# Kernel tuning notes

Hardware: AMD Instinct MI355X
Metric: run time of the kernel (lower is better)

Reference implementation:

```python
import jax, jax.numpy as jnp
import numpy as np

HID = 1024
INTER = 4096
NUM_EXPERTS = 4096
NUM_KEYS = 64  # floor(sqrt(4096))
TOP_K = 8
B, S = 2, 2048


def setup_inputs() -> dict:
    key = jax.random.key(0)
    ks = jax.random.split(key, 7)
    sc = 0.02
    return {
        "hidden_states": jax.random.normal(ks[0], (B, S, HID), jnp.float32),
        "w_gate": jax.random.normal(ks[1], (INTER, HID), jnp.float32) * sc,
        "w_up": jax.random.normal(ks[2], (INTER, HID), jnp.float32) * sc,
        "w_down": jax.random.normal(ks[3], (HID, INTER), jnp.float32) * sc,
        "w_router": jax.random.normal(ks[4], (NUM_KEYS * 2, HID), jnp.float32) * sc,
        "down_embed": jax.random.normal(ks[5], (NUM_EXPERTS, HID), jnp.float32) * sc,
        "up_embed": jax.random.normal(ks[6], (NUM_EXPERTS, HID), jnp.float32) * sc,
    }


def reference(hidden_states, w_gate, w_up, w_down, w_router, down_embed, up_embed):
    b, s, h = hidden_states.shape
    n = b * s
    # router: [b,s,2*nk] -> row-major reshape to (2, n, nk), matching torch .view
    router_logits = (hidden_states @ w_router.T).reshape(2, n, NUM_KEYS)
    # topk with k == nk is a full descending sort (faithful to torch .topk)
    scores_xy, idx_xy = jax.lax.top_k(router_logits, NUM_KEYS)
    scores_x, scores_y = scores_xy[0], scores_xy[1]  # (n, nk) each
    idx_x, idx_y = idx_xy[0], idx_xy[1]
    all_scores = (scores_x[:, :, None] + scores_y[:, None, :]).reshape(n, NUM_KEYS * NUM_KEYS)
    all_indices = (idx_x[:, :, None] * NUM_KEYS + idx_y[:, None, :]).reshape(n, NUM_KEYS * NUM_KEYS)
    scores, pos = jax.lax.top_k(all_scores, TOP_K)  # (n, top_k)
    indices = jnp.take_along_axis(all_indices, pos, axis=-1)
    routing_weights = jax.nn.softmax(scores, axis=-1)
    routing_weights = routing_weights / routing_weights.sum(-1, keepdims=True)  # norm_topk_prob
    de = down_embed[indices]  # (n, top_k, h)
    ue = up_embed[indices]    # (n, top_k, h)
    x_flat = hidden_states.reshape(n, h)
    ew = jnp.einsum('nkh,nh->nk', de, x_flat)
    ew = jax.nn.silu(ew) * routing_weights
    experts_states = jnp.einsum('nk,nkh->nh', ew, ue).reshape(b, s, h)
    mlp = (jax.nn.silu(x_flat @ w_gate.T) * (x_flat @ w_up.T)) @ w_down.T
    out = mlp.reshape(b, s, h) + experts_states
    return (out, router_logits)
```

## Files before the change

### kernel.cpp

```cpp
#include <hip/hip_runtime.h>
#include <hip/hip_bf16.h>
#include <stdint.h>

typedef __bf16 bf16;
typedef __attribute__((ext_vector_type(8))) __bf16 bf16x8;
typedef __attribute__((ext_vector_type(4))) float f32x4;

static constexpr int kTok = 4096;
static constexpr int kHid = 1024;
static constexpr int kInter = 4096;

#define GLDS16(g, l)                                                \
  __builtin_amdgcn_global_load_lds(                                 \
      (const __attribute__((address_space(1))) void*)(g),           \
      (__attribute__((address_space(3))) void*)(l), 16, 0, 0)

__global__ void __launch_bounds__(256) k_cvt_rt(
    const float* X, const float* Wg, const float* Wu, const float* Wd,
    const float* Wr, const float* dE, const float* uE,
    bf16* Xb, bf16* Wgb, bf16* Wub, bf16* Wdb, bf16* dEb, bf16* uEb,
    float* out1) {
  __shared__ bf16 smem[8192];
  const int bid = blockIdx.x;
  const int t = threadIdx.x;

  if (bid < 32) {
    const int w = t >> 6;
    const int L = t & 63;
    const int la = L & 15;
    const int lk = (L >> 4) * 8;
    bf16* sA = smem;
    bf16* sB = smem + 4096;
    const long m0 = (long)bid * 128;
    const int wm = (w >> 1) * 64;
    const int wn = (w & 1) * 64;
    const f32x4 fzero = {0.f, 0.f, 0.f, 0.f};
    f32x4 acc[4][4];
#pragma unroll
    for (int i = 0; i < 4; ++i)
#pragma unroll
      for (int j = 0; j < 4; ++j) acc[i][j] = fzero;

    const int c0 = t, c1 = t + 256;
    const long ar0 = m0 + (c0 >> 2), ar1 = m0 + (c1 >> 2);
    const long br0 = (c0 >> 2), br1 = (c1 >> 2);
    const int ko = (c0 & 3) * 8;
    const bf16* sAr = sA + (wm + la) * 32 + lk;
    const bf16* sBr = sB + (wn + la) * 32 + lk;

    for (int kt = 0; kt < 32; ++kt) {
      const long k0 = (long)kt << 5;
      bf16x8 av0, av1, bv0, bv1;
      {
        const f32x4 x0 = *(const f32x4*)(X + ar0 * kHid + k0 + ko);
        const f32x4 x1 = *(const f32x4*)(X + ar0 * kHid + k0 + ko + 4);
        const f32x4 y0 = *(const f32x4*)(X + ar1 * kHid + k0 + ko);
        const f32x4 y1 = *(const f32x4*)(X + ar1 * kHid + k0 + ko + 4);
        const f32x4 p0 = *(const f32x4*)(Wr + br0 * kHid + k0 + ko);
        const f32x4 p1 = *(const f32x4*)(Wr + br0 * kHid + k0 + ko + 4);
        const f32x4 q0 = *(const f32x4*)(Wr + br1 * kHid + k0 + ko);
        const f32x4 q1 = *(const f32x4*)(Wr + br1 * kHid + k0 + ko + 4);
#pragma unroll
        for (int i = 0; i < 4; ++i) {
          av0[i] = (bf16)x0[i]; av0[4 + i] = (bf16)x1[i];
          av1[i] = (bf16)y0[i]; av1[4 + i] = (bf16)y1[i];
          bv0[i] = (bf16)p0[i]; bv0[4 + i] = (bf16)p1[i];
          bv1[i] = (bf16)q0[i]; bv1[4 + i] = (bf16)q1[i];
        }
      }
      __syncthreads();
      *(bf16x8*)(sA + c0 * 8) = av0;
      *(bf16x8*)(sA + c1 * 8) = av1;
      *(bf16x8*)(sB + c0 * 8) = bv0;
      *(bf16x8*)(sB + c1 * 8) = bv1;
      __syncthreads();
      bf16x8 af[4], bfm[4];
#pragma unroll
      for (int i = 0; i < 4; ++i) {
        af[i] = *(const bf16x8*)(sAr + i * 512);
        bfm[i] = *(const bf16x8*)(sBr + i * 512);
      }
#pragma unroll
      for (int i = 0; i < 4; ++i)
#pragma unroll
        for (int j = 0; j < 4; ++j)
          acc[i][j] = __builtin_amdgcn_mfma_f32_16x16x32_bf16(
              af[i], bfm[j], acc[i][j], 0, 0, 0);
    }
    const long col0 = wn + la;
    const long row0 = m0 + wm + (L >> 4) * 4;
#pragma unroll
    for (int i = 0; i < 4; ++i)
#pragma unroll
      for (int j = 0; j < 4; ++j)
#pragma unroll
        for (int r = 0; r < 4; ++r)
          out1[(row0 + i * 16 + r) * 128 + col0 + j * 16] = acc[i][j][r];
    return;
  }

  if (bid >= 8224) {
    const int c2 = bid - 8224;
    const float* src = (c2 >> 11) ? uE : dE;
    bf16* dst = (c2 >> 11) ? uEb : dEb;
    const long i = ((long)(c2 & 2047) * 256 + t) * 8;
    const f32x4 a = *(const f32x4*)(src + i);
    const f32x4 b = *(const f32x4*)(src + i + 4);
    bf16x8 o;
#pragma unroll
    for (int k = 0; k < 4; ++k) { o[k] = (bf16)a[k]; o[4 + k] = (bf16)b[k]; }
    *(bf16x8*)(dst + i) = o;
    return;
  }

  const int c = bid - 32;
  const float* src;
  bf16* dst;
  switch (c >> 11) {
    case 0: src = X;  dst = Xb;  break;
    case 1: src = Wg; dst = Wgb; break;
    case 2: src = Wu; dst = Wub; break;
    default: src = Wd; dst = Wdb; break;
  }
  const long i = ((long)(c & 2047) * 256 + t) * 8;
  const f32x4 a = *(const f32x4*)(src + i);
  const f32x4 b = *(const f32x4*)(src + i + 4);
  bf16x8 o;
#pragma unroll
  for (int k = 0; k < 4; ++k) { o[k] = (bf16)a[k]; o[4 + k] = (bf16)b[k]; }
  *(bf16x8*)(dst + i) = o;
}

__global__ void __launch_bounds__(256, 2) gemm_gu(
    const bf16* X, const bf16* Wg, const bf16* Wu, bf16* H) {
  constexpr int K = kHid, N = kInter;
  __shared__ bf16 sX[128 * 32];
  __shared__ bf16 sG[128 * 32];
  __shared__ bf16 sU[128 * 32];
  const int t = threadIdx.x;
  const int w = t >> 6;
  const int L = t & 63;
  const long m0 = (long)blockIdx.y * 128;
  const long n0 = (long)blockIdx.x * 128;
  const int wm = (w >> 1) * 64;
  const int wn = (w & 1) * 64;

  f32x4 accG[4][4], accU[4][4];
  const f32x4 fzero = {0.f, 0.f, 0.f, 0.f};
#pragma unroll
  for (int i = 0; i < 4; ++i)
#pragma unroll
    for (int j = 0; j < 4; ++j) { accG[i][j] = fzero; accU[i][j] = fzero; }

  const int r0 = t >> 2;
  const int ko = (t & 3) * 8;
  const bf16* gX0 = X + (m0 + r0) * K + ko;
  const bf16* gX1 = gX0 + (long)64 * K;
  const bf16* gG0 = Wg + (n0 + r0) * K + ko;
  const bf16* gG1 = gG0 + (long)64 * K;
  const bf16* gU0 = Wu + (n0 + r0) * K + ko;
  const bf16* gU1 = gU0 + (long)64 * K;
  bf16* lX0 = sX + w * 512;
  bf16* lX1 = sX + 2048 + w * 512;
  bf16* lG0 = sG + w * 512;
  bf16* lG1 = sG + 2048 + w * 512;
  bf16* lU0 = sU + w * 512;
  bf16* lU1 = sU + 2048 + w * 512;

  const int la = L & 15;
  const int lk = (L >> 4) * 8;
  const bf16* sXr = sX + (wm + la) * 32 + lk;
  const bf16* sGr = sG + (wn + la) * 32 + lk;
  const bf16* sUr = sU + (wn + la) * 32 + lk;

  for (int kt = 0; kt < K / 32; ++kt) {
    const long k0 = (long)kt << 5;
    GLDS16(gX0 + k0, lX0);
    GLDS16(gX1 + k0, lX1);
    GLDS16(gG0 + k0, lG0);
    GLDS16(gG1 + k0, lG1);
    GLDS16(gU0 + k0, lU0);
    GLDS16(gU1 + k0, lU1);
    __syncthreads();
    bf16x8 af[4], bg[4], bu[4];
#pragma unroll
    for (int i = 0; i < 4; ++i) {
      af[i] = *(const bf16x8*)(sXr + i * 512);
      bg[i] = *(const bf16x8*)(sGr + i * 512);
      bu[i] = *(const bf16x8*)(sUr + i * 512);
    }
#pragma unroll
    for (int i = 0; i < 4; ++i)
#pragma unroll
      for (int j = 0; j < 4; ++j) {
        accG[i][j] = __builtin_amdgcn_mfma_f32_16x16x32_bf16(af[i], bg[j],
                                                             accG[i][j], 0, 0, 0);
        accU[i][j] = __builtin_amdgcn_mfma_f32_16x16x32_bf16(af[i], bu[j],
                                                             accU[i][j], 0, 0, 0);
      }
    __syncthreads();
  }
  const long col0 = n0 + wn + la;
  const long row0 = m0 + wm + (L >> 4) * 4;
#pragma unroll
  for (int i = 0; i < 4; ++i)
#pragma unroll
    for (int j = 0; j < 4; ++j)
#pragma unroll
      for (int r = 0; r < 4; ++r) {
        const float g = accG[i][j][r];
        const float u = accU[i][j][r];
        H[(row0 + i * 16 + r) * N + col0 + j * 16] =
            (bf16)(g / (1.f + __expf(-g)) * u);
      }
}

__global__ void __launch_bounds__(256, 2) gemm_down(
    const bf16* Hs, const bf16* Wd, float* out0, float* p1) {
  constexpr int K = kInter, N = kHid;
  __shared__ bf16 sA[128 * 32];
  __shared__ bf16 sB[128 * 32];
  const int t = threadIdx.x;
  const int w = t >> 6;
  const int L = t & 63;
  const long m0 = (long)blockIdx.y * 128;
  const long n0 = (long)blockIdx.x * 128;
  const long zb = (long)blockIdx.z * 2048;
  const int wm = (w >> 1) * 64;
  const int wn = (w & 1) * 64;

  f32x4 acc[4][4];
  const f32x4 fzero = {0.f, 0.f, 0.f, 0.f};
#pragma unroll
  for (int i = 0; i < 4; ++i)
#pragma unroll
    for (int j = 0; j < 4; ++j) acc[i][j] = fzero;

  const int r0 = t >> 2;
  const int ko = (t & 3) * 8;
  const bf16* gA0 = Hs + (m0 + r0) * K + zb + ko;
  const bf16* gA1 = gA0 + (long)64 * K;
  const bf16* gB0 = Wd + (n0 + r0) * K + zb + ko;
  const bf16* gB1 = gB0 + (long)64 * K;
  bf16* lA0 = sA + w * 512;
  bf16* lA1 = sA + 2048 + w * 512;
  bf16* lB0 = sB + w * 512;
  bf16* lB1 = sB + 2048 + w * 512;

  const int la = L & 15;
  const int lk = (L >> 4) * 8;
  const bf16* sAr = sA + (wm + la) * 32 + lk;
  const bf16* sBr = sB + (wn + la) * 32 + lk;

  for (int kt = 0; kt < 64; ++kt) {
    const long k0 = (long)kt << 5;
    GLDS16(gA0 + k0, lA0);
    GLDS16(gA1 + k0, lA1);
    GLDS16(gB0 + k0, lB0);
    GLDS16(gB1 + k0, lB1);
    __syncthreads();
    bf16x8 af[4], bfm[4];
#pragma unroll
    for (int i = 0; i < 4; ++i) {
      af[i] = *(const bf16x8*)(sAr + i * 512);
      bfm[i] = *(const bf16x8*)(sBr + i * 512);
    }
#pragma unroll
    for (int i = 0; i < 4; ++i)
#pragma unroll
      for (int j = 0; j < 4; ++j)
        acc[i][j] = __builtin_amdgcn_mfma_f32_16x16x32_bf16(af[i], bfm[j],
                                                            acc[i][j], 0, 0, 0);
    __syncthreads();
  }
  float* dst = (blockIdx.z == 0) ? out0 : p1;
  const long col0 = n0 + wn + la;
  const long row0 = m0 + wm + (L >> 4) * 4;
#pragma unroll
  for (int i = 0; i < 4; ++i)
#pragma unroll
    for (int j = 0; j < 4; ++j)
#pragma unroll
      for (int r = 0; r < 4; ++r)
        dst[(row0 + i * 16 + r) * N + col0 + j * 16] = acc[i][j][r];
}

template <int BT>
__global__ void __launch_bounds__(256) route_expert(
    const float* __restrict__ logits, const float* __restrict__ X,
    const float* __restrict__ dE, const float* __restrict__ uE,
    const bf16* __restrict__ dEb, const bf16* __restrict__ uEb,
    const float* __restrict__ p1, float* __restrict__ out0) {
  __shared__ float s_vals[2][128];
  __shared__ int s_idx[2][128];
  __shared__ float s_acc[2][16][64];
  const int w = threadIdx.x >> 6;
  const int L = threadIdx.x & 63;
  const int tok = w >> 1;
  const int h = w & 1;
  const int j = blockIdx.x * 2 + tok;

  const int half = (j & 1) * 64;
  const int rx = j >> 1;
  const float vx = logits[(long)rx * 128 + half + L];
  const float vy = logits[(long)(2048 + rx) * 128 + half + L];

  int rkx = 0, rky = 0;
  for (int m = 0; m < 64; ++m) {
    const float mx = __shfl(vx, m);
    const float my = __shfl(vy, m);
    rkx += (mx > vx) || (mx == vx && m < L);
    rky += (my > vy) || (my == vy && m < L);
  }
  rkx &= 63;
  rky &= 63;
  s_vals[tok][rkx] = vx;
  s_idx[tok][rkx] = L;
  s_vals[tok][64 + rky] = vy;
  s_idx[tok][64 + rky] = L;
  __syncthreads();

  int p = 0, q = 0;
  const bool valid = (L < 20);
  if (L < 8)       { p = L;      q = 0; }
  else if (L < 12) { p = L - 8;  q = 1; }
  else if (L < 14) { p = L - 12; q = 2; }
  else if (L < 16) { p = L - 14; q = 3; }
  else if (L < 20) { p = 0;      q = L - 12; }
  const float kNegBig = -3.0e38f;
  float myv = valid ? (s_vals[tok][p] + s_vals[tok][64 + q]) : kNegBig;
  int mypos = valid ? (p * 64 + q) : 0x7fffffff;

  float topv[8];
  int tope[8];
#pragma unroll
  for (int r = 0; r < 8; ++r) {
    float bv = myv;
    int bp = mypos;
#pragma unroll
    for (int d = 32; d > 0; d >>= 1) {
      const float ov = __shfl_xor(bv, d);
      const int op = __shfl_xor(bp, d);
      if (ov > bv || (ov == bv && op < bp)) { bv = ov; bp = op; }
    }
    topv[r] = bv;
    const int pp = (bp >> 6) & 127, qq = bp & 63;
    tope[r] = (s_idx[tok][pp] * 64 + s_idx[tok][64 + qq]) & 4095;
    if (mypos == bp) myv = kNegBig;
  }

  float e[8], wsum = 0.f;
#pragma unroll
  for (int r = 0; r < 8; ++r) {
    e[r] = __expf(topv[r] - topv[0]);
    wsum += e[r];
  }
  const float winv = 1.f / wsum;

  const long xoff = (long)j * kHid + L * 16;
  float xv[16], acc[16];
#pragma unroll
  for (int v4 = 0; v4 < 4; ++v4) {
    const f32x4 xl = *(const f32x4*)(X + xoff + v4 * 4);
#pragma unroll
    for (int i = 0; i < 4; ++i) { xv[v4 * 4 + i] = xl[i]; acc[v4 * 4 + i] = 0.f; }
  }

  const long lo16 = (long)L * 16;
  if (BT) {
    const long eo0 = (long)tope[h * 4 + 0] * kHid + lo16;
    const long eo1 = (long)tope[h * 4 + 1] * kHid + lo16;
    const long eo2 = (long)tope[h * 4 + 2] * kHid + lo16;
    const long eo3 = (long)tope[h * 4 + 3] * kHid + lo16;
    const bf16x8 d00 = *(const bf16x8*)(dEb + eo0);
    const bf16x8 d01 = *(const bf16x8*)(dEb + eo0 + 8);
    const bf16x8 d10 = *(const bf16x8*)(dEb + eo1);
    const bf16x8 d11 = *(const bf16x8*)(dEb + eo1 + 8);
    const bf16x8 d20 = *(const bf16x8*)(dEb + eo2);
    const bf16x8 d21 = *(const bf16x8*)(dEb + eo2 + 8);
    const bf16x8 d30 = *(const bf16x8*)(dEb + eo3);
    const bf16x8 d31 = *(const bf16x8*)(dEb + eo3 + 8);
    const bf16x8 u00 = *(const bf16x8*)(uEb + eo0);
    const bf16x8 u01 = *(const bf16x8*)(uEb + eo0 + 8);
    const bf16x8 u10 = *(const bf16x8*)(uEb + eo1);
    const bf16x8 u11 = *(const bf16x8*)(uEb + eo1 + 8);
    const bf16x8 u20 = *(const bf16x8*)(uEb + eo2);
    const bf16x8 u21 = *(const bf16x8*)(uEb + eo2 + 8);
    const bf16x8 u30 = *(const bf16x8*)(uEb + eo3);
    const bf16x8 u31 = *(const bf16x8*)(uEb + eo3 + 8);

    float d0 = 0.f, d1 = 0.f, d2 = 0.f, d3 = 0.f;
#pragma unroll
    for (int i = 0; i < 8; ++i) {
      d0 += (float)d00[i] * xv[i] + (float)d01[i] * xv[8 + i];
      d1 += (float)d10[i] * xv[i] + (float)d11[i] * xv[8 + i];
      d2 += (float)d20[i] * xv[i] + (float)d21[i] * xv[8 + i];
      d3 += (float)d30[i] * xv[i] + (float)d31[i] * xv[8 + i];
    }
#pragma unroll
    for (int dd = 32; dd > 0; dd >>= 1) {
      d0 += __shfl_xor(d0, dd);
      d1 += __shfl_xor(d1, dd);
      d2 += __shfl_xor(d2, dd);
      d3 += __shfl_xor(d3, dd);
    }
    const float w0 = d0 / (1.f + __expf(-d0)) * (e[h * 4 + 0] * winv);
    const float w1 = d1 / (1.f + __expf(-d1)) * (e[h * 4 + 1] * winv);
    const float w2 = d2 / (1.f + __expf(-d2)) * (e[h * 4 + 2] * winv);
    const float w3 = d3 / (1.f + __expf(-d3)) * (e[h * 4 + 3] * winv);
#pragma unroll
    for (int i = 0; i < 8; ++i) {
      acc[i]     += w0 * (float)u00[i] + w1 * (float)u10[i] +
                    w2 * (float)u20[i] + w3 * (float)u30[i];
      acc[8 + i] += w0 * (float)u01[i] + w1 * (float)u11[i] +
                    w2 * (float)u21[i] + w3 * (float)u31[i];
    }
  } else {
    long eoA = (long)tope[h * 4 + 0] * kHid + lo16;
    f32x4 dA0 = *(const f32x4*)(dE + eoA);
    f32x4 dA1 = *(const f32x4*)(dE + eoA + 4);
    f32x4 dA2 = *(const f32x4*)(dE + eoA + 8);
    f32x4 dA3 = *(const f32x4*)(dE + eoA + 12);
    f32x4 uA0 = *(const f32x4*)(uE + eoA);
    f32x4 uA1 = *(const f32x4*)(uE + eoA + 4);
    f32x4 uA2 = *(const f32x4*)(uE + eoA + 8);
    f32x4 uA3 = *(const f32x4*)(uE + eoA + 12);
#pragma unroll
    for (int r = 0; r < 4; ++r) {
      f32x4 dB0, dB1, dB2, dB3, uB0, uB1, uB2, uB3;
      if (r < 3) {
        const long eoB = (long)tope[h * 4 + r + 1] * kHid + lo16;
        dB0 = *(const f32x4*)(dE + eoB);
        dB1 = *(const f32x4*)(dE + eoB + 4);
        dB2 = *(const f32x4*)(dE + eoB + 8);
        dB3 = *(const f32x4*)(dE + eoB + 12);
        uB0 = *(const f32x4*)(uE + eoB);
        uB1 = *(const f32x4*)(uE + eoB + 4);
        uB2 = *(const f32x4*)(uE + eoB + 8);
        uB3 = *(const f32x4*)(uE + eoB + 12);
      }
      float d = 0.f;
#pragma unroll
      for (int i = 0; i < 4; ++i) {
        d += dA0[i] * xv[i];
        d += dA1[i] * xv[4 + i];
        d += dA2[i] * xv[8 + i];
        d += dA3[i] * xv[12 + i];
      }
#pragma unroll
      for (int dd = 32; dd > 0; dd >>= 1) d += __shfl_xor(d, dd);
      const float ew = d / (1.f + __expf(-d)) * (e[h * 4 + r] * winv);
#pragma unroll
      for (int i = 0; i < 4; ++i) {
        acc[i]      += ew * uA0[i];
        acc[4 + i]  += ew * uA1[i];
        acc[8 + i]  += ew * uA2[i];
        acc[12 + i] += ew * uA3[i];
      }
      if (r < 3) {
        dA0 = dB0; dA1 = dB1; dA2 = dB2; dA3 = dB3;
        uA0 = uB0; uA1 = uB1; uA2 = uB2; uA3 = uB3;
      }
    }
  }

  if (h == 1) {
#pragma unroll
    for (int k = 0; k < 16; ++k) s_acc[tok][k][L] = acc[k];
  }
  __syncthreads();
  if (h == 0) {
#pragma unroll
    for (int k = 0; k < 16; ++k) acc[k] += s_acc[tok][k][L];
    float* po = out0 + xoff;
    const float* pp1 = p1 + xoff;
#pragma unroll
    for (int v4 = 0; v4 < 4; ++v4) {
      f32x4 ov = *(const f32x4*)(po + v4 * 4);
      const f32x4 pv = *(const f32x4*)(pp1 + v4 * 4);
#pragma unroll
      for (int i = 0; i < 4; ++i) ov[i] += pv[i] + acc[v4 * 4 + i];
      *(f32x4*)(po + v4 * 4) = ov;
    }
  }
}

extern "C" void kernel_launch(void* const* d_in, const int* in_sizes, int n_in,
                              void* d_out, int out_size, void* d_ws,
                              size_t ws_size, hipStream_t stream) {
  (void)in_sizes; (void)n_in; (void)out_size;
  const float* X  = (const float*)d_in[0];
  const float* Wg = (const float*)d_in[1];
  const float* Wu = (const float*)d_in[2];
  const float* Wd = (const float*)d_in[3];
  const float* Wr = (const float*)d_in[4];
  const float* dE = (const float*)d_in[5];
  const float* uE = (const float*)d_in[6];

  float* out0 = (float*)d_out;
  float* out1 = out0 + (size_t)kTok * kHid;

  bf16* wsH = (bf16*)d_ws;
  bf16* Xb  = wsH + (size_t)kTok * kInter;
  bf16* Wgb = Xb  + (size_t)kTok * kHid;
  bf16* Wub = Wgb + (size_t)kInter * kHid;
  bf16* Wdb = Wub + (size_t)kInter * kHid;
  float* p1 = (float*)Xb;
  const bool bigws = ws_size >= (size_t)80 * 1024 * 1024;
  bf16* dEb = (bf16*)((char*)d_ws + (size_t)64 * 1024 * 1024);
  bf16* uEb = (bf16*)((char*)d_ws + (size_t)72 * 1024 * 1024);

  dim3 blk(256);
  const int cvt_blocks = bigws ? 12320 : 8224;
  k_cvt_rt<<<dim3(cvt_blocks), blk, 0, stream>>>(
      X, Wg, Wu, Wd, Wr, dE, uE, Xb, Wgb, Wub, Wdb, dEb, uEb, out1);
  gemm_gu<<<dim3(32, 32), blk, 0, stream>>>(Xb, Wgb, Wub, wsH);
  gemm_down<<<dim3(8, 32, 2), blk, 0, stream>>>(wsH, Wdb, out0, p1);
  if (bigws)
    route_expert<1><<<dim3(kTok / 2), blk, 0, stream>>>(out1, X, dE, uE, dEb,
                                                        uEb, p1, out0);
  else
    route_expert<0><<<dim3(kTok / 2), blk, 0, stream>>>(out1, X, dE, uE, dEb,
                                                        uEb, p1, out0);
}
```

Baseline: 323.5 us.

## Restructure gate/up GEMM into 1024-thread double-buffered pipelined kernel

The fused gate/up GEMM moves from 256-thread 128x128 tiles with a single-stage K loop to 1024-thread 256x128 tiles with a K step of 64. Shared memory is double-buffered, and staging loads for the next tile are interleaved between MFMA phases, using explicit vmcnt waits, barriers and setprio. The goal is to hide global-to-LDS latency behind compute and to reuse the weight tiles across more rows. In exchange, each block uses more LDS and registers, and the hand-tuned waitcnt counts must match the exact order of issued loads.

```diff
diff --git a/kernel.cpp b/kernel.cpp
--- a/kernel.cpp
+++ b/kernel.cpp
@@ -14,6 +14,11 @@
   __builtin_amdgcn_global_load_lds(                                 \
       (const __attribute__((address_space(1))) void*)(g),           \
       (__attribute__((address_space(3))) void*)(l), 16, 0, 0)
+
+#define WAIT_BAR(N)                                     \
+  asm volatile("s_waitcnt vmcnt(" #N ")" ::: "memory"); \
+  __builtin_amdgcn_s_barrier();                         \
+  __builtin_amdgcn_sched_barrier(0)
 
 __global__ void __launch_bounds__(256) k_cvt_rt(
     const float* X, const float* Wg, const float* Wu, const float* Wd,
@@ -131,86 +136,111 @@
   *(bf16x8*)(dst + i) = o;
 }
 
-__global__ void __launch_bounds__(256, 2) gemm_gu(
-    const bf16* X, const bf16* Wg, const bf16* Wu, bf16* H) {
-  constexpr int K = kHid, N = kInter;
-  __shared__ bf16 sX[128 * 32];
-  __shared__ bf16 sG[128 * 32];
-  __shared__ bf16 sU[128 * 32];
+__global__ void __launch_bounds__(1024, 1) gemm_gu(
+    const bf16* __restrict__ X, const bf16* __restrict__ Wg,
+    const bf16* __restrict__ Wu, bf16* __restrict__ H) {
+  constexpr int K = kHid;
+  constexpr int NT = K / 64;
+  __shared__ bf16 sX[2][2][8192];
+  __shared__ bf16 sG[2][8192];
+  __shared__ bf16 sU[2][8192];
   const int t = threadIdx.x;
-  const int w = t >> 6;
+  const int wid = t >> 6;
   const int L = t & 63;
-  const long m0 = (long)blockIdx.y * 128;
+  const int wm = wid >> 2;
+  const int wn = wid & 3;
+  const long m0 = (long)blockIdx.y * 256;
   const long n0 = (long)blockIdx.x * 128;
-  const int wm = (w >> 1) * 64;
-  const int wn = (w & 1) * 64;
-
-  f32x4 accG[4][4], accU[4][4];
+
+  f32x4 accG[4][2], accU[4][2];
   const f32x4 fzero = {0.f, 0.f, 0.f, 0.f};
 #pragma unroll
   for (int i = 0; i < 4; ++i)
 #pragma unroll
-    for (int j = 0; j < 4; ++j) { accG[i][j] = fzero; accU[i][j] = fzero; }
-
-  const int r0 = t >> 2;
-  const int ko = (t & 3) * 8;
-  const bf16* gX0 = X + (m0 + r0) * K + ko;
-  const bf16* gX1 = gX0 + (long)64 * K;
-  const bf16* gG0 = Wg + (n0 + r0) * K + ko;
-  const bf16* gG1 = gG0 + (long)64 * K;
-  const bf16* gU0 = Wu + (n0 + r0) * K + ko;
-  const bf16* gU1 = gU0 + (long)64 * K;
-  bf16* lX0 = sX + w * 512;
-  bf16* lX1 = sX + 2048 + w * 512;
-  bf16* lG0 = sG + w * 512;
-  bf16* lG1 = sG + 2048 + w * 512;
-  bf16* lU0 = sU + w * 512;
-  bf16* lU1 = sU + 2048 + w * 512;
+    for (int j = 0; j < 2; ++j) { accG[i][j] = fzero; accU[i][j] = fzero; }
+
+  const bf16* gX = X + (m0 + wid * 16 + (L >> 2)) * K + (L & 3) * 8;
+  const bf16* gG = Wg + (n0 + wid * 8 + (L >> 3)) * K + (L & 7) * 8;
+  const bf16* gU = Wu + (n0 + wid * 8 + (L >> 3)) * K + (L & 7) * 8;
+  const int lo = wid * 512;
+
+#define STG_X(b_, h_, kt_) GLDS16(gX + (kt_) * 64 + (h_) * 32, &sX[b_][h_][lo])
+#define STG_G(b_, kt_)     GLDS16(gG + (kt_) * 64, &sG[b_][lo])
+#define STG_U(b_, kt_)     GLDS16(gU + (kt_) * 64, &sU[b_][lo])
 
   const int la = L & 15;
   const int lk = (L >> 4) * 8;
-  const bf16* sXr = sX + (wm + la) * 32 + lk;
-  const bf16* sGr = sG + (wn + la) * 32 + lk;
-  const bf16* sUr = sU + (wn + la) * 32 + lk;
-
-  for (int kt = 0; kt < K / 32; ++kt) {
-    const long k0 = (long)kt << 5;
-    GLDS16(gX0 + k0, lX0);
-    GLDS16(gX1 + k0, lX1);
-    GLDS16(gG0 + k0, lG0);
-    GLDS16(gG1 + k0, lG1);
-    GLDS16(gU0 + k0, lU0);
-    GLDS16(gU1 + k0, lU1);
-    __syncthreads();
-    bf16x8 af[4], bg[4], bu[4];
-#pragma unroll
-    for (int i = 0; i < 4; ++i) {
-      af[i] = *(const bf16x8*)(sXr + i * 512);
-      bg[i] = *(const bf16x8*)(sGr + i * 512);
-      bu[i] = *(const bf16x8*)(sUr + i * 512);
-    }
-#pragma unroll
-    for (int i = 0; i < 4; ++i)
-#pragma unroll
-      for (int j = 0; j < 4; ++j) {
-        accG[i][j] = __builtin_amdgcn_mfma_f32_16x16x32_bf16(af[i], bg[j],
-                                                             accG[i][j], 0, 0, 0);
-        accU[i][j] = __builtin_amdgcn_mfma_f32_16x16x32_bf16(af[i], bu[j],
-                                                             accU[i][j], 0, 0, 0);
-      }
-    __syncthreads();
-  }
-  const long col0 = n0 + wn + la;
-  const long row0 = m0 + wm + (L >> 4) * 4;
+  const int roA = (wm * 64 + la) * 32 + lk;
+  const int roB = (wn * 32 + la) * 64 + lk;
+
+  STG_X(0, 0, 0);
+  STG_G(0, 0);
+  STG_X(0, 1, 0);
+  STG_U(0, 0);
+
+#define PH_LOAD_A(b_, ks_)                                   \
+  _Pragma("unroll") for (int i = 0; i < 4; ++i)              \
+      af[i] = *(const bf16x8*)(&sX[b_][ks_][roA] + i * 512);
+#define PH_LOAD_B(dst_, s_, b_, ks_)                         \
+  _Pragma("unroll") for (int j = 0; j < 2; ++j)              \
+      dst_[j] = *(const bf16x8*)(&s_[b_][roB + (ks_) * 32] + j * 1024);
+#define PH_MFMA(accM, bM)                                    \
+  __builtin_amdgcn_s_setprio(1);                             \
+  _Pragma("unroll") for (int i = 0; i < 4; ++i)              \
+      _Pragma("unroll") for (int j = 0; j < 2; ++j)          \
+          accM[i][j] = __builtin_amdgcn_mfma_f32_16x16x32_bf16( \
+              af[i], bM[j], accM[i][j], 0, 0, 0);            \
+  __builtin_amdgcn_s_setprio(0)
+
+  for (int kt = 0; kt < NT - 1; ++kt) {
+    const int b = kt & 1;
+    const int nb = b ^ 1;
+    bf16x8 af[4], bg[2], bu[2];
+    WAIT_BAR(2);
+    PH_LOAD_A(b, 0);
+    PH_LOAD_B(bg, sG, b, 0);
+    STG_X(nb, 0, kt + 1);
+    PH_MFMA(accG, bg);
+    WAIT_BAR(1);
+    PH_LOAD_B(bu, sU, b, 0);
+    STG_G(nb, kt + 1);
+    PH_MFMA(accU, bu);
+    PH_LOAD_A(b, 1);
+    PH_LOAD_B(bg, sG, b, 1);
+    STG_X(nb, 1, kt + 1);
+    PH_MFMA(accG, bg);
+    PH_LOAD_B(bu, sU, b, 1);
+    STG_U(nb, kt + 1);
+    PH_MFMA(accU, bu);
+  }
+  {
+    const int b = (NT - 1) & 1;
+    bf16x8 af[4], bg[2], bu[2];
+    WAIT_BAR(2);
+    PH_LOAD_A(b, 0);
+    PH_LOAD_B(bg, sG, b, 0);
+    PH_MFMA(accG, bg);
+    WAIT_BAR(0);
+    PH_LOAD_B(bu, sU, b, 0);
+    PH_MFMA(accU, bu);
+    PH_LOAD_A(b, 1);
+    PH_LOAD_B(bg, sG, b, 1);
+    PH_MFMA(accG, bg);
+    PH_LOAD_B(bu, sU, b, 1);
+    PH_MFMA(accU, bu);
+  }
+
+  const long col0 = n0 + wn * 32 + la;
+  const long row0 = m0 + wm * 64 + (L >> 4) * 4;
 #pragma unroll
   for (int i = 0; i < 4; ++i)
 #pragma unroll
-    for (int j = 0; j < 4; ++j)
+    for (int j = 0; j < 2; ++j)
 #pragma unroll
       for (int r = 0; r < 4; ++r) {
         const float g = accG[i][j][r];
         const float u = accU[i][j][r];
-        H[(row0 + i * 16 + r) * N + col0 + j * 16] =
+        H[(row0 + i * 16 + r) * kInter + col0 + j * 16] =
             (bf16)(g / (1.f + __expf(-g)) * u);
       }
 }
@@ -514,7 +544,7 @@
   const int cvt_blocks = bigws ? 12320 : 8224;
   k_cvt_rt<<<dim3(cvt_blocks), blk, 0, stream>>>(
       X, Wg, Wu, Wd, Wr, dE, uE, Xb, Wgb, Wub, Wdb, dEb, uEb, out1);
-  gemm_gu<<<dim3(32, 32), blk, 0, stream>>>(Xb, Wgb, Wub, wsH);
+  gemm_gu<<<dim3(32, 16), dim3(1024), 0, stream>>>(Xb, Wgb, Wub, wsH);
   gemm_down<<<dim3(8, 32, 2), blk, 0, stream>>>(wsH, Wdb, out0, p1);
   if (bigws)
     route_expert<1><<<dim3(kTok / 2), blk, 0, stream>>>(out1, X, dE, uE, dEb,
```

After: 314.9 us. -2.7%, faster.
